# Performance work log

Measured on AMD Instinct MI355X. Metric: run time of the kernel, lower is better.

The kernel has to match this reference:

```python
import jax, jax.numpy as jnp
import numpy as np

N_NODES = 100000
N_EDGES = 1200000
IN_FEATS = 128
HIDDEN = 64
OUT_FEATS = 40


def setup_inputs() -> dict:
    key = jax.random.key(0)
    k1, k2, k3, k4, k5 = jax.random.split(key, 5)
    x = jax.random.normal(k1, (N_NODES, IN_FEATS), dtype=jnp.float32)
    edge_index = jax.random.randint(k2, (2, N_EDGES), 0, N_NODES, dtype=jnp.int64)
    W1 = jax.random.normal(k3, (IN_FEATS, HIDDEN), dtype=jnp.float32) * (1.0 / np.sqrt(IN_FEATS))
    b1 = jnp.zeros((HIDDEN,), dtype=jnp.float32)
    W2 = jax.random.normal(k4, (HIDDEN, HIDDEN), dtype=jnp.float32) * (1.0 / np.sqrt(HIDDEN))
    b2 = jnp.zeros((HIDDEN,), dtype=jnp.float32)
    Wc = jax.random.normal(k5, (HIDDEN, OUT_FEATS), dtype=jnp.float32) * (1.0 / np.sqrt(HIDDEN))
    bc = jnp.zeros((OUT_FEATS,), dtype=jnp.float32)
    return {"x": x, "edge_index": edge_index, "W1": W1, "b1": b1,
            "W2": W2, "b2": b2, "Wc": Wc, "bc": bc}


def _gcn_norm(edge_index, n_nodes):
    # add self-loops, then symmetric normalization deg^{-1/2}[src] * deg^{-1/2}[dst]
    loops = jnp.arange(n_nodes, dtype=edge_index.dtype)
    src = jnp.concatenate([edge_index[0], loops])
    dst = jnp.concatenate([edge_index[1], loops])
    ones = jnp.ones(src.shape[0], dtype=jnp.float32)
    deg = jax.ops.segment_sum(ones, dst, num_segments=n_nodes)  # in-degree incl. self-loop
    dinv = jnp.where(deg > 0, jax.lax.rsqrt(deg), 0.0)
    norm = dinv[src] * dinv[dst]  # [E+N]
    return src, dst, norm


def _gcn_conv(h, W, b, src, dst, norm, n_nodes):
    h = h @ W                          # [N, F_out] dense transform first (PyG GCNConv)
    msg = h[src] * norm[:, None]       # gather + normalize, [E+N, F_out]
    out = jax.ops.segment_sum(msg, dst, num_segments=n_nodes)  # scatter-add
    return out + b


def reference(x, edge_index, W1, b1, W2, b2, Wc, bc):
    n = x.shape[0]
    src, dst, norm = _gcn_norm(edge_index, n)
    # dropout is identity in eval mode
    h = jax.nn.relu(_gcn_conv(x, W1, b1, src, dst, norm, n))
    embedding = _gcn_conv(h, W2, b2, src, dst, norm, n)
    logits = embedding @ Wc + bc
    soft_label = jax.nn.softmax(logits, axis=1)
    hard_label = jnp.argmax(soft_label, axis=1)
    return (logits, embedding, soft_label, hard_label)
```

## Files before the change

kernel.cpp:

```cpp
#include <hip/hip_runtime.h>
#include <hip/hip_bf16.h>
#include <math.h>

typedef __hip_bfloat16 bf16;

__device__ __forceinline__ float loadf(const void* p, size_t i, bool f32m) {
    return f32m ? ((const float*)p)[i]
                : __bfloat162float(((const bf16*)p)[i]);
}
__device__ __forceinline__ void storef(void* p, size_t i, float v, bool f32m) {
    if (f32m) ((float*)p)[i] = v;
    else      ((bf16*)p)[i] = __float2bfloat16(v);
}
__device__ __forceinline__ int ldidx(const int* w, size_t e, bool e64, size_t E, int row) {
    return e64 ? w[2 * (row * E + e)] : w[row * E + e];
}

__global__ void k_detect(const void* x, const int* ei, float* flags) {
    int lane = threadIdx.x;
    const unsigned short* hx = (const unsigned short*)x;
    unsigned short u = hx[2 * lane];
    int ex = (u >> 7) & 0xFF;
    bool tame = (ex >= 117 && ex <= 136);
    unsigned long long mt = __ballot(tame);
    unsigned long long mz = __ballot(ei[2 * lane + 1] != 0);
    if (lane == 0) {
        flags[0] = (__popcll(mt) >= 48) ? 0.0f : 1.0f;
        flags[1] = (mz == 0ULL) ? 1.0f : 0.0f;
    }
}


__global__ void k_zero_small(int* __restrict__ p, int m) {
    int i = blockIdx.x * 256 + threadIdx.x;
    if (i < m) p[i] = 0;
}

#define SCB_EPT 16

__global__ __launch_bounds__(256) void k_bucket_hist(const int* __restrict__ ei,
                                                     const float* __restrict__ flags,
                                                     int* __restrict__ bcnt, int E, int NB) {
    __shared__ int lcnt[512];
    bool e64 = flags[1] > 0.5f;
    int tid = threadIdx.x;
    for (int i = tid; i < NB; i += 256) lcnt[i] = 0;
    __syncthreads();
    int base = blockIdx.x * 256 * SCB_EPT;
#pragma unroll
    for (int j = 0; j < SCB_EPT; ++j) {
        int e = base + j * 256 + tid;
        if (e < E) atomicAdd(&lcnt[ldidx(ei, e, e64, E, 1) >> 8], 1);
    }
    __syncthreads();
    for (int i = tid; i < NB; i += 256) {
        int c = lcnt[i];
        if (c) atomicAdd(&bcnt[i], c);
    }
}

__global__ __launch_bounds__(512) void k_scan_buckets(const int* __restrict__ bcnt,
                                                      int* __restrict__ bbase,
                                                      int* __restrict__ bcur, int NB) {
    __shared__ int sh[512];
    int tid = threadIdx.x;
    int v = (tid < NB) ? bcnt[tid] : 0;
    sh[tid] = v;
    __syncthreads();
    for (int off = 1; off < 512; off <<= 1) {
        int t = (tid >= off) ? sh[tid - off] : 0;
        __syncthreads();
        sh[tid] += t;
        __syncthreads();
    }
    if (tid < NB) {
        int ex = sh[tid] - v;
        bbase[tid] = ex;
        bcur[tid] = ex;
    }
    if (tid == 0) bbase[NB] = sh[511];
}

__global__ __launch_bounds__(256) void k_bucket_scatter(const int* __restrict__ ei,
                                                        const float* __restrict__ flags,
                                                        int* __restrict__ bcur,
                                                        int2* __restrict__ recs,
                                                        int E, int NB) {
    __shared__ int lcnt[512], lrank[512], lbase[512];
    bool e64 = flags[1] > 0.5f;
    int tid = threadIdx.x;
    for (int i = tid; i < NB; i += 256) { lcnt[i] = 0; lrank[i] = 0; }
    __syncthreads();
    int base = blockIdx.x * 256 * SCB_EPT;
    int s[SCB_EPT], d[SCB_EPT];
#pragma unroll
    for (int j = 0; j < SCB_EPT; ++j) {
        int e = base + j * 256 + tid;
        if (e < E) {
            s[j] = ldidx(ei, e, e64, E, 0);
            d[j] = ldidx(ei, e, e64, E, 1);
            atomicAdd(&lcnt[d[j] >> 8], 1);
        } else d[j] = -1;
    }
    __syncthreads();
    for (int i = tid; i < NB; i += 256) {
        int c = lcnt[i];
        lbase[i] = c ? atomicAdd(&bcur[i], c) : 0;
    }
    __syncthreads();
#pragma unroll
    for (int j = 0; j < SCB_EPT; ++j) {
        if (d[j] >= 0) {
            int b = d[j] >> 8;
            int r = atomicAdd(&lrank[b], 1);
            recs[lbase[b] + r] = make_int2(s[j], d[j]);
        }
    }
}

__global__ __launch_bounds__(256) void k_bucket_csr(const int2* __restrict__ recs,
                                                    const int* __restrict__ bbase,
                                                    int* __restrict__ rowptr,
                                                    float* __restrict__ dinv,
                                                    int* __restrict__ srcs,
                                                    int n, int E) {
    __shared__ int lcnt[256];
    __shared__ int lcur[256];
    int b = blockIdx.x, tid = threadIdx.x;
    int e0 = bbase[b], e1 = bbase[b + 1];
    lcnt[tid] = 0;
    __syncthreads();
    for (int i = e0 + tid; i < e1; i += 256)
        atomicAdd(&lcnt[recs[i].y & 255], 1);
    __syncthreads();
    int c = lcnt[tid];
    lcur[tid] = c;
    __syncthreads();
    for (int off = 1; off < 256; off <<= 1) {
        int t = (tid >= off) ? lcur[tid - off] : 0;
        __syncthreads();
        lcur[tid] += t;
        __syncthreads();
    }
    int rp = bbase[b] + lcur[tid] - c;
    int node = (b << 8) + tid;
    if (node < n) {
        rowptr[node] = rp;
        dinv[node] = rsqrtf((float)(c + 1));
    }
    lcur[tid] = rp;
    __syncthreads();
    for (int i = e0 + tid; i < e1; i += 256) {
        int2 r = recs[i];
        int pos = atomicAdd(&lcur[r.y & 255], 1);
        srcs[pos] = r.x;
    }
    if (b == 0 && tid == 0) rowptr[n] = E;
}

template <int K, bool XF32>
__global__ __launch_bounds__(256) void k_gemm3(const void* __restrict__ Xa,
                                               const void* __restrict__ Xb,
                                               const void* __restrict__ W,
                                               const float* __restrict__ flags,
                                               const float* __restrict__ rowscale,
                                               float* __restrict__ out, int n) {
    __shared__ float xs[64 * (K + 4)];
    __shared__ float wl[K * 68];
    bool f32m = flags[0] > 0.5f;
    const void* X = f32m ? Xa : Xb;
    bool xf32 = XF32 || f32m;
    int tid = threadIdx.x;
    int r0 = blockIdx.x * 64;

    if (f32m) {
        for (int i = tid * 4; i < K * 64; i += 1024) {
            int k = i >> 6, cc = i & 63;
            float4 v = *(const float4*)((const float*)W + i);
            *(float4*)&wl[k * 68 + cc] = v;
        }
    } else {
        for (int i = tid; i < K * 64; i += 256) {
            int k = i >> 6, cc = i & 63;
            wl[k * 68 + cc] = __bfloat162float(((const bf16*)W)[i]);
        }
    }
    if (xf32) {
        for (int i = tid * 4; i < 64 * K; i += 1024) {
            int row = i / K, k = i % K;
            float4 v = {0, 0, 0, 0};
            if (r0 + row < n) v = *(const float4*)((const float*)X + (size_t)(r0 + row) * K + k);
            *(float4*)&xs[row * (K + 4) + k] = v;
        }
    } else {
        for (int i = tid * 4; i < 64 * K; i += 1024) {
            int row = i / K, k = i % K;
            float4 v = {0, 0, 0, 0};
            if (r0 + row < n) {
                const bf16* p = (const bf16*)X + (size_t)(r0 + row) * K + k;
                v.x = __bfloat162float(p[0]); v.y = __bfloat162float(p[1]);
                v.z = __bfloat162float(p[2]); v.w = __bfloat162float(p[3]);
            }
            *(float4*)&xs[row * (K + 4) + k] = v;
        }
    }
    __syncthreads();

    int lane = tid & 63, wv = tid >> 6;
    int rg = lane >> 4, cg = lane & 15;
    int rbase = wv * 16 + rg * 4;
    int cbase = cg * 4;

    float acc[4][4];
#pragma unroll
    for (int r = 0; r < 4; ++r)
#pragma unroll
        for (int c = 0; c < 4; ++c) acc[r][c] = 0.0f;

#pragma unroll 2
    for (int k = 0; k < K; k += 4) {
        float4 xrv[4], wv4[4];
#pragma unroll
        for (int r = 0; r < 4; ++r)
            xrv[r] = *(const float4*)&xs[(rbase + r) * (K + 4) + k];
#pragma unroll
        for (int j = 0; j < 4; ++j)
            wv4[j] = *(const float4*)&wl[(k + j) * 68 + cbase];
#pragma unroll
        for (int r = 0; r < 4; ++r) {
            const float* xp = (const float*)&xrv[r];
#pragma unroll
            for (int j = 0; j < 4; ++j) {
                float xv = xp[j];
                acc[r][0] += xv * wv4[j].x;
                acc[r][1] += xv * wv4[j].y;
                acc[r][2] += xv * wv4[j].z;
                acc[r][3] += xv * wv4[j].w;
            }
        }
    }

#pragma unroll
    for (int r = 0; r < 4; ++r) {
        int row = r0 + rbase + r;
        if (row < n) {
            float sc = rowscale[row];
            float4 st = {acc[r][0] * sc, acc[r][1] * sc, acc[r][2] * sc, acc[r][3] * sc};
            *(float4*)&out[(size_t)row * 64 + cbase] = st;
        }
    }
}

template <int EP>
__global__ __launch_bounds__(256) void k_agg(const float* __restrict__ t,
                                             const float* __restrict__ dinv,
                                             const int* __restrict__ rowptr,
                                             const int* __restrict__ srcs,
                                             const void* __restrict__ bias,
                                             const float* __restrict__ flags,
                                             void* __restrict__ d_out, size_t emb_base,
                                             float* __restrict__ B_ws, int n) {
    bool f32m = flags[0] > 0.5f;
    int wid = (blockIdx.x * 256 + threadIdx.x) >> 6;
    int lane = threadIdx.x & 63;
    if (wid >= n) return;
    float dv = dinv[wid];
    float acc = t[(size_t)wid * 64 + lane];
    int e0 = rowptr[wid], e1 = rowptr[wid + 1];
    for (int base = e0; base < e1; base += 64) {
        int m = e1 - base; if (m > 64) m = 64;
        int idx = base + lane;
        int s_l = (idx < e1) ? srcs[idx] : 0;
        int j = 0;
        for (; j + 8 <= m; j += 8) {
            int s0 = __shfl(s_l, j + 0, 64), s1 = __shfl(s_l, j + 1, 64);
            int s2 = __shfl(s_l, j + 2, 64), s3 = __shfl(s_l, j + 3, 64);
            int s4 = __shfl(s_l, j + 4, 64), s5 = __shfl(s_l, j + 5, 64);
            int s6 = __shfl(s_l, j + 6, 64), s7 = __shfl(s_l, j + 7, 64);
            float v0 = t[(size_t)s0 * 64 + lane];
            float v1 = t[(size_t)s1 * 64 + lane];
            float v2 = t[(size_t)s2 * 64 + lane];
            float v3 = t[(size_t)s3 * 64 + lane];
            float v4 = t[(size_t)s4 * 64 + lane];
            float v5 = t[(size_t)s5 * 64 + lane];
            float v6 = t[(size_t)s6 * 64 + lane];
            float v7 = t[(size_t)s7 * 64 + lane];
            acc += ((v0 + v1) + (v2 + v3)) + ((v4 + v5) + (v6 + v7));
        }
        for (; j < m; ++j) {
            int s = __shfl(s_l, j, 64);
            acc += t[(size_t)s * 64 + lane];
        }
    }
    acc = acc * dv + loadf(bias, lane, f32m);
    size_t oi = (size_t)wid * 64 + lane;
    if (EP == 0) acc = fmaxf(acc, 0.0f);
    if (f32m) {
        ((float*)d_out)[emb_base + oi] = acc;
    } else {
        B_ws[oi] = acc;
        if (EP == 1) ((bf16*)d_out)[emb_base + oi] = __float2bfloat16(acc);
    }
}


__device__ __forceinline__ void store_row40(void* out, size_t base, const float* a, bool f32m) {
    if (f32m) {
        float4* p = (float4*)((float*)out + base);
#pragma unroll
        for (int q = 0; q < 10; ++q) {
            float4 st = {a[q * 4 + 0], a[q * 4 + 1], a[q * 4 + 2], a[q * 4 + 3]};
            p[q] = st;
        }
    } else {
        __hip_bfloat162* p = (__hip_bfloat162*)((bf16*)out + base);
#pragma unroll
        for (int i = 0; i < 20; ++i) {
            __hip_bfloat162 h;
            h.x = __float2bfloat16(a[2 * i]);
            h.y = __float2bfloat16(a[2 * i + 1]);
            p[i] = h;
        }
    }
}

__global__ __launch_bounds__(256) void k_classifier(const float* __restrict__ flags,
                                                    const void* __restrict__ Wc,
                                                    const void* __restrict__ bc,
                                                    void* __restrict__ out,
                                                    size_t emb_base, size_t soft_base,
                                                    size_t hard_base,
                                                    const float* __restrict__ B_ws,
                                                    int n) {
    __shared__ __align__(16) float wcs[64 * 40];
    __shared__ __align__(16) float bcs[40];
    bool f32m = flags[0] > 0.5f;
    const float* emb = f32m ? ((const float*)out + emb_base) : B_ws;
    int tid = threadIdx.x;

    if (f32m) {
        for (int i = tid * 4; i < 64 * 40; i += 1024)
            *(float4*)&wcs[i] = *(const float4*)((const float*)Wc + i);
    } else {
        for (int i = tid; i < 64 * 40; i += 256)
            wcs[i] = __bfloat162float(((const bf16*)Wc)[i]);
    }
    if (tid < 40) bcs[tid] = loadf(bc, tid, f32m);
    __syncthreads();

    int node = blockIdx.x * 256 + tid;
    if (node >= n) return;

    float acc[40];
#pragma unroll
    for (int q = 0; q < 10; ++q) {
        float4 b4 = *(const float4*)&bcs[q * 4];
        acc[q * 4 + 0] = b4.x; acc[q * 4 + 1] = b4.y;
        acc[q * 4 + 2] = b4.z; acc[q * 4 + 3] = b4.w;
    }

    const float4* erow = (const float4*)(emb + (size_t)node * 64);
#pragma unroll 2
    for (int j = 0; j < 16; ++j) {
        float4 e4 = erow[j];
        float ev[4] = {e4.x, e4.y, e4.z, e4.w};
#pragma unroll
        for (int kk = 0; kk < 4; ++kk) {
            float e = ev[kk];
            const float4* wr = (const float4*)&wcs[(j * 4 + kk) * 40];
#pragma unroll
            for (int q = 0; q < 10; ++q) {
                float4 w = wr[q];
                acc[q * 4 + 0] = fmaf(e, w.x, acc[q * 4 + 0]);
                acc[q * 4 + 1] = fmaf(e, w.y, acc[q * 4 + 1]);
                acc[q * 4 + 2] = fmaf(e, w.z, acc[q * 4 + 2]);
                acc[q * 4 + 3] = fmaf(e, w.w, acc[q * 4 + 3]);
            }
        }
    }

    store_row40(out, (size_t)node * 40, acc, f32m);

    float m0 = acc[0], m1 = acc[1], m2 = acc[2], m3 = acc[3];
#pragma unroll
    for (int q = 1; q < 10; ++q) {
        m0 = fmaxf(m0, acc[q * 4 + 0]); m1 = fmaxf(m1, acc[q * 4 + 1]);
        m2 = fmaxf(m2, acc[q * 4 + 2]); m3 = fmaxf(m3, acc[q * 4 + 3]);
    }
    float m = fmaxf(fmaxf(m0, m1), fmaxf(m2, m3));

    int bi = 63;
#pragma unroll
    for (int c = 0; c < 40; ++c)
        if (acc[c] == m && c < bi) bi = c;

    float s = 0.0f;
#pragma unroll
    for (int c = 0; c < 40; ++c) {
        float e = expf(acc[c] - m);
        acc[c] = e;
        s += e;
    }
    float rs = 1.0f / s;
#pragma unroll
    for (int c = 0; c < 40; ++c) acc[c] *= rs;

    store_row40(out, soft_base + (size_t)node * 40, acc, f32m);
    storef(out, hard_base + node, (float)bi, f32m);
}

extern "C" void kernel_launch(void* const* d_in, const int* in_sizes, int n_in,
                              void* d_out, int out_size, void* d_ws, size_t ws_size,
                              hipStream_t stream) {
    const void* x  = d_in[0];
    const int*  ei = (const int*)d_in[1];
    const void* W1 = d_in[2];
    const void* b1 = d_in[3];
    const void* W2 = d_in[4];
    const void* b2 = d_in[5];
    const void* Wc = d_in[6];
    const void* bc = d_in[7];

    const int n = in_sizes[0] / 128;
    const int E = in_sizes[1] / 2;
    const int NB = (n + 255) / 256;

    float* ws    = (float*)d_ws;
    const size_t npad = (((size_t)n + 1023) / 1024) * 1024;
    const size_t Epad = (((size_t)E + 255) / 256) * 256;
    float* flags  = ws;
    int*   bcnt   = (int*)(ws + 256);
    int*   bbase  = (int*)(ws + 768);
    int*   bcur   = (int*)(ws + 1536);
    int*   rowptr = (int*)(ws + 2048);
    float* dinv   = (float*)(rowptr + npad);
    int*   srcs   = (int*)(dinv + npad);
    float* A      = (float*)(srcs + Epad);
    float* B_ws   = A + (size_t)n * 64;
    int2*  recs   = (int2*)B_ws;

    const size_t emb_base  = (size_t)n * 40;
    const size_t soft_base = (size_t)n * 104;
    const size_t hard_base = (size_t)n * 144;
    float* h1_f32m = (float*)d_out + emb_base;

    const int gS  = (E + 256 * SCB_EPT - 1) / (256 * SCB_EPT);
    const int gG  = (n + 63) / 64;
    const int gW  = (n + 3) / 4;
    const int gC  = (n + 255) / 256;

    k_detect<<<1, 64, 0, stream>>>(x, ei, flags);

    k_zero_small<<<2, 256, 0, stream>>>(bcnt, 512);
    k_bucket_hist<<<gS, 256, 0, stream>>>(ei, flags, bcnt, E, NB);
    k_scan_buckets<<<1, 512, 0, stream>>>(bcnt, bbase, bcur, NB);
    k_bucket_scatter<<<gS, 256, 0, stream>>>(ei, flags, bcur, recs, E, NB);
    k_bucket_csr<<<NB, 256, 0, stream>>>(recs, bbase, rowptr, dinv, srcs, n, E);

    k_gemm3<128, false><<<gG, 256, 0, stream>>>(x, x, W1, flags, dinv, A, n);
    k_agg<0><<<gW, 256, 0, stream>>>(A, dinv, rowptr, srcs, b1, flags,
                                     d_out, emb_base, B_ws, n);

    k_gemm3<64, true><<<gG, 256, 0, stream>>>(h1_f32m, B_ws, W2, flags, dinv, A, n);
    k_agg<1><<<gW, 256, 0, stream>>>(A, dinv, rowptr, srcs, b2, flags,
                                     d_out, emb_base, B_ws, n);

    k_classifier<<<gC, 256, 0, stream>>>(flags, Wc, bc, d_out,
                                         emb_base, soft_base, hard_base, B_ws, n);
}
```

Baseline: 342.4 us.

## Aggregate two nodes per wavefront with float4 gathers across four lane groups

The GCN aggregation kernel now gives each 64-lane wavefront two destination nodes instead of one. Lanes split into four groups of 16, and each lane gathers a float4 slice of a neighbor row, so every wave load fetches four neighbor rows per node. Partial sums are combined across the groups with xor shuffles, and the self-loop is treated as an extra neighbor. The aim is wider, more parallel memory requests and fewer waves; the cost is extra shuffles and idle lanes when the two nodes' degrees differ.

```diff
diff --git a/kernel.cpp b/kernel.cpp
--- a/kernel.cpp
+++ b/kernel.cpp
@@ -261,45 +261,112 @@
                                              void* __restrict__ d_out, size_t emb_base,
                                              float* __restrict__ B_ws, int n) {
     bool f32m = flags[0] > 0.5f;
-    int wid = (blockIdx.x * 256 + threadIdx.x) >> 6;
+    int wvid = (blockIdx.x * 256 + threadIdx.x) >> 6;
     int lane = threadIdx.x & 63;
-    if (wid >= n) return;
-    float dv = dinv[wid];
-    float acc = t[(size_t)wid * 64 + lane];
-    int e0 = rowptr[wid], e1 = rowptr[wid + 1];
-    for (int base = e0; base < e1; base += 64) {
-        int m = e1 - base; if (m > 64) m = 64;
-        int idx = base + lane;
-        int s_l = (idx < e1) ? srcs[idx] : 0;
-        int j = 0;
-        for (; j + 8 <= m; j += 8) {
-            int s0 = __shfl(s_l, j + 0, 64), s1 = __shfl(s_l, j + 1, 64);
-            int s2 = __shfl(s_l, j + 2, 64), s3 = __shfl(s_l, j + 3, 64);
-            int s4 = __shfl(s_l, j + 4, 64), s5 = __shfl(s_l, j + 5, 64);
-            int s6 = __shfl(s_l, j + 6, 64), s7 = __shfl(s_l, j + 7, 64);
-            float v0 = t[(size_t)s0 * 64 + lane];
-            float v1 = t[(size_t)s1 * 64 + lane];
-            float v2 = t[(size_t)s2 * 64 + lane];
-            float v3 = t[(size_t)s3 * 64 + lane];
-            float v4 = t[(size_t)s4 * 64 + lane];
-            float v5 = t[(size_t)s5 * 64 + lane];
-            float v6 = t[(size_t)s6 * 64 + lane];
-            float v7 = t[(size_t)s7 * 64 + lane];
-            acc += ((v0 + v1) + (v2 + v3)) + ((v4 + v5) + (v6 + v7));
-        }
-        for (; j < m; ++j) {
-            int s = __shfl(s_l, j, 64);
-            acc += t[(size_t)s * 64 + lane];
-        }
-    }
-    acc = acc * dv + loadf(bias, lane, f32m);
-    size_t oi = (size_t)wid * 64 + lane;
-    if (EP == 0) acc = fmaxf(acc, 0.0f);
+    int grp = lane >> 4;
+    int col4 = lane & 15;
+    int v0 = wvid * 2;
+    int v1 = v0 + 1;
+    if (v0 >= n) return;
+    bool has1 = (v1 < n);
+
+    float4 bias4;
     if (f32m) {
-        ((float*)d_out)[emb_base + oi] = acc;
+        bias4 = ((const float4*)bias)[col4];
     } else {
-        B_ws[oi] = acc;
-        if (EP == 1) ((bf16*)d_out)[emb_base + oi] = __float2bfloat16(acc);
+        const bf16* bp = (const bf16*)bias + col4 * 4;
+        bias4.x = __bfloat162float(bp[0]); bias4.y = __bfloat162float(bp[1]);
+        bias4.z = __bfloat162float(bp[2]); bias4.w = __bfloat162float(bp[3]);
+    }
+
+    float dvA = dinv[v0];
+    float dvB = has1 ? dinv[v1] : 0.0f;
+    int e0a = rowptr[v0], e1a = rowptr[v0 + 1];
+    int e0b = has1 ? rowptr[v1] : 0;
+    int e1b = has1 ? rowptr[v1 + 1] : 0;
+    int degA = e1a - e0a + 1;
+    int degB = has1 ? (e1b - e0b + 1) : 0;
+    int degMax = degA > degB ? degA : degB;
+
+    float4 accA = {0, 0, 0, 0}, accB = {0, 0, 0, 0};
+
+    for (int base = 0; base < degMax; base += 64) {
+        int jA = base + lane;
+        int sA_l = -1;
+        if (jA == 0) sA_l = v0;
+        else if (jA < degA) sA_l = srcs[e0a + jA - 1];
+        int sB_l = -1;
+        if (has1) {
+            int jB = base + lane;
+            if (jB == 0) sB_l = v1;
+            else if (jB < degB) sB_l = srcs[e0b + jB - 1];
+        }
+        int rem = degMax - base;
+        int mq = rem < 64 ? rem : 64;
+
+        for (int q = 0; q < mq; q += 16) {
+            int sa[4], sb[4];
+#pragma unroll
+            for (int u = 0; u < 4; ++u) {
+                int idx = q + 4 * u + grp;
+                sa[u] = __shfl(sA_l, idx, 64);
+                sb[u] = __shfl(sB_l, idx, 64);
+            }
+            float4 va[4], vb[4];
+#pragma unroll
+            for (int u = 0; u < 4; ++u) {
+                va[u] = make_float4(0, 0, 0, 0);
+                if (sa[u] >= 0)
+                    va[u] = *((const float4*)(t + ((size_t)sa[u] << 6)) + col4);
+                vb[u] = make_float4(0, 0, 0, 0);
+                if (sb[u] >= 0)
+                    vb[u] = *((const float4*)(t + ((size_t)sb[u] << 6)) + col4);
+            }
+#pragma unroll
+            for (int u = 0; u < 4; ++u) {
+                accA.x += va[u].x; accA.y += va[u].y; accA.z += va[u].z; accA.w += va[u].w;
+                accB.x += vb[u].x; accB.y += vb[u].y; accB.z += vb[u].z; accB.w += vb[u].w;
+            }
+        }
+    }
+
+#pragma unroll
+    for (int off = 16; off < 64; off <<= 1) {
+        accA.x += __shfl_xor(accA.x, off, 64);
+        accA.y += __shfl_xor(accA.y, off, 64);
+        accA.z += __shfl_xor(accA.z, off, 64);
+        accA.w += __shfl_xor(accA.w, off, 64);
+        accB.x += __shfl_xor(accB.x, off, 64);
+        accB.y += __shfl_xor(accB.y, off, 64);
+        accB.z += __shfl_xor(accB.z, off, 64);
+        accB.w += __shfl_xor(accB.w, off, 64);
+    }
+
+    int v = -1; float4 acc; float dv = 0.0f;
+    if (grp == 0) { v = v0; acc = accA; dv = dvA; }
+    else if (grp == 1 && has1) { v = v1; acc = accB; dv = dvB; }
+    if (v >= 0) {
+        acc.x = acc.x * dv + bias4.x;
+        acc.y = acc.y * dv + bias4.y;
+        acc.z = acc.z * dv + bias4.z;
+        acc.w = acc.w * dv + bias4.w;
+        if (EP == 0) {
+            acc.x = fmaxf(acc.x, 0.0f); acc.y = fmaxf(acc.y, 0.0f);
+            acc.z = fmaxf(acc.z, 0.0f); acc.w = fmaxf(acc.w, 0.0f);
+        }
+        size_t ob = (size_t)v * 64 + col4 * 4;
+        if (f32m) {
+            *(float4*)((float*)d_out + emb_base + ob) = acc;
+        } else {
+            *(float4*)&B_ws[ob] = acc;
+            if (EP == 1) {
+                __hip_bfloat162 h0, h1;
+                h0.x = __float2bfloat16(acc.x); h0.y = __float2bfloat16(acc.y);
+                h1.x = __float2bfloat16(acc.z); h1.y = __float2bfloat16(acc.w);
+                __hip_bfloat162* p = (__hip_bfloat162*)((bf16*)d_out + emb_base + ob);
+                p[0] = h0; p[1] = h1;
+            }
+        }
     }
 }
 
@@ -446,7 +513,7 @@
 
     const int gS  = (E + 256 * SCB_EPT - 1) / (256 * SCB_EPT);
     const int gG  = (n + 63) / 64;
-    const int gW  = (n + 3) / 4;
+    const int gW  = (n + 7) / 8;
     const int gC  = (n + 255) / 256;
 
     k_detect<<<1, 64, 0, stream>>>(x, ei, flags);
```

Result: faster. 326.5 us (-4.7%).
